# Kernel optimization log

Hardware: AMD Instinct MI355X
Metric: run time of the kernel (lower is better)

Reference implementation:

```python
import jax, jax.numpy as jnp
import numpy as np
import math

B, H, LQ, LK, D = 2, 16, 2048, 2048, 128

def setup_inputs() -> dict:
    key = jax.random.key(0)
    kq, kk, kv, km = jax.random.split(key, 4)
    return {
        "query": jax.random.normal(kq, (B, H, LQ, D), dtype=jnp.float32),
        "key": jax.random.normal(kk, (B, H, LK, D), dtype=jnp.float32),
        "value": jax.random.normal(kv, (B, H, LK, D), dtype=jnp.float32),
        # positive integer multiplicities in [1, 8] so log() is finite
        "key_multiplicities": jax.random.randint(km, (B, LK), 1, 9, dtype=jnp.int32),
    }

def reference(query, key, value, key_multiplicities):
    scale = 1.0 / math.sqrt(query.shape[-1])
    # scores: [B, H, Lq, Lk]
    scores = jnp.einsum("bhqd,bhkd->bhqk", query, key) * scale
    # additive log-multiplicity bias, broadcast over heads and queries
    log_mult = jnp.log(key_multiplicities.astype(scores.dtype))  # [B, Lk]
    scores = scores + log_mult[:, None, None, :]
    attn = jax.nn.softmax(scores, axis=-1)
    # dropout_p = 0.0 -> identity
    return jnp.einsum("bhqk,bhkd->bhqd", attn, value)
```

## Files before the change

### kernel.cpp

```cpp
#include <hip/hip_runtime.h>
#include <hip/hip_bf16.h>

constexpr int B_  = 2;
constexpr int H_  = 16;
constexpr int LQ_ = 2048;
constexpr int LK_ = 2048;
constexpr int D_  = 128;

constexpr int BM = 128;
constexpr int BN = 64;
constexpr int NT = LK_ / BN;
constexpr int TILE_SH = 64 * 128;

constexpr float SCALE_LOG2E = 0.12751649734586414f;

typedef short s16x4 __attribute__((ext_vector_type(4)));
typedef short s16x8 __attribute__((ext_vector_type(8)));
typedef float f32x4 __attribute__((ext_vector_type(4)));

#define MFMA16 __builtin_amdgcn_mfma_f32_16x16x32_bf16

#if __has_builtin(__builtin_amdgcn_exp2f)
#define EXP2(x) __builtin_amdgcn_exp2f(x)
#else
#define EXP2(x) exp2f(x)
#endif
#if __has_builtin(__builtin_amdgcn_logf)
#define LOG2(x) __builtin_amdgcn_logf(x)
#else
#define LOG2(x) log2f(x)
#endif

static __device__ __forceinline__ int pk2bf(float a, float b) {
  float2 t{a, b};
  __hip_bfloat162 h = __float22bfloat162_rn(t);
  return *reinterpret_cast<int*>(&h);
}

static __device__ __forceinline__ void dma16(const short* g, short* l) {
  __builtin_amdgcn_global_load_lds(
      (const __attribute__((address_space(1))) void*)g,
      (__attribute__((address_space(3))) void*)l, 16, 0, 0);
}

__global__ __launch_bounds__(256)
void prep(const float* __restrict__ kg, const float* __restrict__ vg,
          const int* __restrict__ multg, short* __restrict__ wsK,
          short* __restrict__ wsV, float* __restrict__ wsBias) {
  __shared__ float tileF[64 * 133];
  const int tid = threadIdx.x;
  const int wg  = blockIdx.x;
  const float* kp = kg + (size_t)wg * 64 * 128;
  const float* vp = vg + (size_t)wg * 64 * 128;
  short* wk = wsK + (size_t)wg * TILE_SH;
  short* wv = wsV + (size_t)wg * TILE_SH;

#pragma unroll
  for (int i = 0; i < 4; ++i) {
    int idx = tid + i * 256;
    int row = idx >> 4, blk = idx & 15;
    const float* src = kp + row * 128 + blk * 8;
    float4 a = *(const float4*)src;
    float4 c4 = *(const float4*)(src + 4);
    int4 t;
    t.x = pk2bf(a.x, a.y);  t.y = pk2bf(a.z, a.w);
    t.z = pk2bf(c4.x, c4.y); t.w = pk2bf(c4.z, c4.w);
    int pos = blk ^ (row & 15);
    *(int4*)&wk[row * 128 + pos * 8] = t;
  }

#pragma unroll
  for (int i = 0; i < 8; ++i) {
    int idx = tid + i * 256;
    int key = idx >> 5, d0 = (idx & 31) * 4;
    float4 a = *(const float4*)(vp + key * 128 + d0);
    float* dst = &tileF[key * 133 + d0];
    dst[0] = a.x; dst[1] = a.y; dst[2] = a.z; dst[3] = a.w;
  }
  __syncthreads();
#pragma unroll
  for (int i = 0; i < 4; ++i) {
    int idx = tid + i * 256;
    int d = idx >> 3, kgrp = idx & 7;
    float v[8];
#pragma unroll
    for (int j = 0; j < 8; ++j) v[j] = tileF[(kgrp * 8 + j) * 133 + d];
    int4 t;
    t.x = pk2bf(v[0], v[1]); t.y = pk2bf(v[2], v[3]);
    t.z = pk2bf(v[4], v[5]); t.w = pk2bf(v[6], v[7]);
    int pos = kgrp ^ ((d >> 1) & 7);
    *(int4*)&wv[d * 64 + pos * 8] = t;
  }

  if (wg < 8) {
    int b = wg >> 2;
    for (int j = tid; j < 512; j += 256) {
      int i0 = (wg & 3) * 512 + j;
      wsBias[b * LK_ + i0] = LOG2((float)multg[b * LK_ + i0]);
    }
  }
}

__global__ __launch_bounds__(256, 2)
void attn_fwd(const float* __restrict__ qg, const short* __restrict__ wsK,
              const short* __restrict__ wsV, const float* __restrict__ wsBias,
              float* __restrict__ outg) {
  __shared__ alignas(16) short Kbuf[2][TILE_SH];
  __shared__ alignas(16) short Vbuf[2][TILE_SH];
  __shared__ alignas(16) short Psh[128 * 64];

  const int tid  = threadIdx.x;
  const int w    = tid >> 6;
  const int lane = tid & 63;
  const int c    = lane & 15;
  const int qd   = lane >> 4;

  const int L   = blockIdx.y * gridDim.x + blockIdx.x;
  const int k8  = L >> 3;
  const int qb  = k8 & 15;
  const int bh  = (L & 7) * 4 + (k8 >> 4);
  const int b   = bh >> 4;

  const float* qptr = qg + (size_t)bh * LQ_ * D_;
  float*       optr = outg + (size_t)bh * LQ_ * D_;
  const short* kws  = wsK + (size_t)bh * NT * TILE_SH;
  const short* vws  = wsV + (size_t)bh * NT * TILE_SH;
  const float* bias = wsBias + b * LK_;

  const int q0 = qb * BM + w * 32;
  s16x8 qf[2][4];
#pragma unroll
  for (int qs = 0; qs < 2; ++qs) {
    const float* qrow = qptr + (size_t)(q0 + qs * 16 + c) * D_ + qd * 8;
#pragma unroll
    for (int kf = 0; kf < 4; ++kf) {
      float4 a  = *(const float4*)(qrow + kf * 32);
      float4 bq = *(const float4*)(qrow + kf * 32 + 4);
      int4 t;
      t.x = pk2bf(a.x * SCALE_LOG2E, a.y * SCALE_LOG2E);
      t.y = pk2bf(a.z * SCALE_LOG2E, a.w * SCALE_LOG2E);
      t.z = pk2bf(bq.x * SCALE_LOG2E, bq.y * SCALE_LOG2E);
      t.w = pk2bf(bq.z * SCALE_LOG2E, bq.w * SCALE_LOG2E);
      qf[qs][kf] = *(s16x8*)&t;
    }
  }

  f32x4 o[2][8];
  float m_r[2], l_r[2];
#pragma unroll
  for (int qs = 0; qs < 2; ++qs) {
#pragma unroll
    for (int dt = 0; dt < 8; ++dt) o[qs][dt] = (f32x4){0.f, 0.f, 0.f, 0.f};
    m_r[qs] = -INFINITY; l_r[qs] = 0.f;
  }

  auto dmaKV = [&](int kt, int bb) {
    const short* gK = kws + (size_t)kt * TILE_SH;
    const short* gV = vws + (size_t)kt * TILE_SH;
#pragma unroll
    for (int i = 0; i < 4; ++i) {
      int off = (w * 4 + i) * 512;
      dma16(gK + off + lane * 8, &Kbuf[bb][off]);
      dma16(gV + off + lane * 8, &Vbuf[bb][off]);
    }
  };

  dmaKV(0, 0);
  __syncthreads();

  for (int kt = 0; kt < NT; ++kt) {
    const int cur = kt & 1;
    if (kt + 1 < NT) dmaKV(kt + 1, cur ^ 1);

    float bvf[4][4];
#pragma unroll
    for (int ct = 0; ct < 4; ++ct) {
      float4 bv = *(const float4*)&bias[kt * BN + ct * 16 + qd * 4];
      bvf[ct][0] = bv.x; bvf[ct][1] = bv.y; bvf[ct][2] = bv.z; bvf[ct][3] = bv.w;
    }

    f32x4 St[2][4];
#pragma unroll
    for (int qs = 0; qs < 2; ++qs)
#pragma unroll
      for (int ct = 0; ct < 4; ++ct) St[qs][ct] = (f32x4){0.f, 0.f, 0.f, 0.f};

#pragma unroll
    for (int ct = 0; ct < 4; ++ct) {
      const short* kb = &Kbuf[cur][(ct * 16 + c) * 128];
#pragma unroll
      for (int kf = 0; kf < 4; ++kf) {
        s16x8 kfr = *(const s16x8*)&kb[((kf * 4 + qd) ^ c) * 8];
        St[0][ct] = MFMA16(kfr, qf[0][kf], St[0][ct], 0, 0, 0);
        St[1][ct] = MFMA16(kfr, qf[1][kf], St[1][ct], 0, 0, 0);
      }
    }

#pragma unroll
    for (int qs = 0; qs < 2; ++qs) {
      float x[4][4];
#pragma unroll
      for (int ct = 0; ct < 4; ++ct)
#pragma unroll
        for (int reg = 0; reg < 4; ++reg)
          x[ct][reg] = St[qs][ct][reg] + bvf[ct][reg];

      float mx = x[0][0];
#pragma unroll
      for (int ct = 0; ct < 4; ++ct)
#pragma unroll
        for (int reg = 0; reg < 4; ++reg) mx = fmaxf(mx, x[ct][reg]);
      mx = fmaxf(mx, __shfl_xor(mx, 16));
      mx = fmaxf(mx, __shfl_xor(mx, 32));

      float mn    = fmaxf(m_r[qs], mx);
      float alpha = EXP2(m_r[qs] - mn);
      m_r[qs] = mn;

      float rs = 0.f;
#pragma unroll
      for (int ct = 0; ct < 4; ++ct)
#pragma unroll
        for (int reg = 0; reg < 4; ++reg) {
          float p = EXP2(x[ct][reg] - mn);
          x[ct][reg] = p;
          rs += p;
        }
      rs += __shfl_xor(rs, 16);
      rs += __shfl_xor(rs, 32);
      l_r[qs] = l_r[qs] * alpha + rs;

      const int pr = w * 32 + qs * 16 + c;
#pragma unroll
      for (int ct = 0; ct < 4; ++ct) {
        int2 pk;
        pk.x = pk2bf(x[ct][0], x[ct][1]);
        pk.y = pk2bf(x[ct][2], x[ct][3]);
        int pos = (ct * 2 + (qd >> 1)) ^ (pr & 7);
        *(int2*)&Psh[pr * 64 + pos * 8 + (qd & 1) * 4] = pk;
      }

      float ar[4];
#pragma unroll
      for (int reg = 0; reg < 4; ++reg) ar[reg] = __shfl(alpha, qd * 4 + reg);
#pragma unroll
      for (int dt = 0; dt < 8; ++dt)
#pragma unroll
        for (int reg = 0; reg < 4; ++reg) o[qs][dt][reg] *= ar[reg];
    }

    s16x8 pf[2][2];
#pragma unroll
    for (int qs = 0; qs < 2; ++qs) {
      const int pr = w * 32 + qs * 16 + c;
#pragma unroll
      for (int kf = 0; kf < 2; ++kf) {
        int pos = (kf * 4 + qd) ^ (pr & 7);
        pf[qs][kf] = *(const s16x8*)&Psh[pr * 64 + pos * 8];
      }
    }
#pragma unroll
    for (int dt = 0; dt < 8; ++dt) {
      int d = dt * 16 + c;
      const short* vb = &Vbuf[cur][d * 64];
      s16x8 vf[2];
#pragma unroll
      for (int kf = 0; kf < 2; ++kf)
        vf[kf] = *(const s16x8*)&vb[((kf * 4 + qd) ^ ((d >> 1) & 7)) * 8];
#pragma unroll
      for (int qs = 0; qs < 2; ++qs)
#pragma unroll
        for (int kf = 0; kf < 2; ++kf)
          o[qs][dt] = MFMA16(pf[qs][kf], vf[kf], o[qs][dt], 0, 0, 0);
    }

    __syncthreads();
  }

#pragma unroll
  for (int qs = 0; qs < 2; ++qs) {
    float lr[4];
#pragma unroll
    for (int reg = 0; reg < 4; ++reg) lr[reg] = __shfl(l_r[qs], qd * 4 + reg);
#pragma unroll
    for (int reg = 0; reg < 4; ++reg) {
      float inv = 1.0f / lr[reg];
      int row = q0 + qs * 16 + qd * 4 + reg;
      float* orow = optr + (size_t)row * D_ + c;
#pragma unroll
      for (int dt = 0; dt < 8; ++dt) orow[dt * 16] = o[qs][dt][reg] * inv;
    }
  }
}

extern "C" void kernel_launch(void* const* d_in, const int* in_sizes, int n_in,
                              void* d_out, int out_size, void* d_ws, size_t ws_size,
                              hipStream_t stream) {
  const float* q = (const float*)d_in[0];
  const float* k = (const float*)d_in[1];
  const float* v = (const float*)d_in[2];
  const int* mult = (const int*)d_in[3];
  float* out = (float*)d_out;

  constexpr size_t KV_BYTES = (size_t)B_ * H_ * LK_ * D_ * 2;
  short* wsK = (short*)d_ws;
  short* wsV = (short*)((char*)d_ws + KV_BYTES);
  float* wsBias = (float*)((char*)d_ws + 2 * KV_BYTES);

  prep<<<dim3(B_ * H_ * NT), dim3(256), 0, stream>>>(k, v, mult, wsK, wsV, wsBias);

  dim3 grid(LQ_ / BM, B_ * H_);
  attn_fwd<<<grid, dim3(256), 0, stream>>>(q, wsK, wsV, wsBias, out);
}
```

Measured before the change: 231.9 us.

## Switch attention to 32x32x16 MFMA with register-resident P and lazy rescaling

Replaces the 16x16x32 MFMA tiling with 32x32x16 MFMAs, computing transposed scores so the probability tile can be turned into the PV operand with permlane32 swaps. This removes the shared-memory round trip for P. The bias is folded into the accumulator init. Output rescaling is skipped unless the running max grows by more than a threshold, which saves the multiply on most tiles at the cost of a looser numerical bound. MFMA sections are wrapped in s_setprio.

After: 213.9 us. 1.08x faster.

```diff
diff --git a/kernel.cpp b/kernel.cpp
--- a/kernel.cpp
+++ b/kernel.cpp
@@ -13,12 +13,12 @@
 constexpr int TILE_SH = 64 * 128;
 
 constexpr float SCALE_LOG2E = 0.12751649734586414f;
-
-typedef short s16x4 __attribute__((ext_vector_type(4)));
+constexpr float DEFER_THR   = 8.0f;
+
 typedef short s16x8 __attribute__((ext_vector_type(8)));
-typedef float f32x4 __attribute__((ext_vector_type(4)));
-
-#define MFMA16 __builtin_amdgcn_mfma_f32_16x16x32_bf16
+typedef float f32x16 __attribute__((ext_vector_type(16)));
+
+#define MFMA32 __builtin_amdgcn_mfma_f32_32x32x16_bf16
 
 #if __has_builtin(__builtin_amdgcn_exp2f)
 #define EXP2(x) __builtin_amdgcn_exp2f(x)
@@ -107,13 +107,12 @@
               float* __restrict__ outg) {
   __shared__ alignas(16) short Kbuf[2][TILE_SH];
   __shared__ alignas(16) short Vbuf[2][TILE_SH];
-  __shared__ alignas(16) short Psh[128 * 64];
 
   const int tid  = threadIdx.x;
   const int w    = tid >> 6;
   const int lane = tid & 63;
-  const int c    = lane & 15;
-  const int qd   = lane >> 4;
+  const int lq   = lane & 31;
+  const int hi   = lane >> 5;
 
   const int L   = blockIdx.y * gridDim.x + blockIdx.x;
   const int k8  = L >> 3;
@@ -128,31 +127,29 @@
   const float* bias = wsBias + b * LK_;
 
   const int q0 = qb * BM + w * 32;
-  s16x8 qf[2][4];
-#pragma unroll
-  for (int qs = 0; qs < 2; ++qs) {
-    const float* qrow = qptr + (size_t)(q0 + qs * 16 + c) * D_ + qd * 8;
-#pragma unroll
-    for (int kf = 0; kf < 4; ++kf) {
-      float4 a  = *(const float4*)(qrow + kf * 32);
-      float4 bq = *(const float4*)(qrow + kf * 32 + 4);
+
+  s16x8 qf[8];
+  {
+    const float* qrow = qptr + (size_t)(q0 + lq) * D_ + hi * 8;
+#pragma unroll
+    for (int kf = 0; kf < 8; ++kf) {
+      float4 a = *(const float4*)(qrow + kf * 16);
+      float4 c = *(const float4*)(qrow + kf * 16 + 4);
       int4 t;
       t.x = pk2bf(a.x * SCALE_LOG2E, a.y * SCALE_LOG2E);
       t.y = pk2bf(a.z * SCALE_LOG2E, a.w * SCALE_LOG2E);
-      t.z = pk2bf(bq.x * SCALE_LOG2E, bq.y * SCALE_LOG2E);
-      t.w = pk2bf(bq.z * SCALE_LOG2E, bq.w * SCALE_LOG2E);
-      qf[qs][kf] = *(s16x8*)&t;
-    }
-  }
-
-  f32x4 o[2][8];
-  float m_r[2], l_r[2];
-#pragma unroll
-  for (int qs = 0; qs < 2; ++qs) {
-#pragma unroll
-    for (int dt = 0; dt < 8; ++dt) o[qs][dt] = (f32x4){0.f, 0.f, 0.f, 0.f};
-    m_r[qs] = -INFINITY; l_r[qs] = 0.f;
-  }
+      t.z = pk2bf(c.x * SCALE_LOG2E, c.y * SCALE_LOG2E);
+      t.w = pk2bf(c.z * SCALE_LOG2E, c.w * SCALE_LOG2E);
+      qf[kf] = *(s16x8*)&t;
+    }
+  }
+
+  f32x16 o[4];
+#pragma unroll
+  for (int dt = 0; dt < 4; ++dt)
+#pragma unroll
+    for (int r = 0; r < 16; ++r) o[dt][r] = 0.f;
+  float m_r = -INFINITY, l_r = 0.f;
 
   auto dmaKV = [&](int kt, int bb) {
     const short* gK = kws + (size_t)kt * TILE_SH;
@@ -172,125 +169,113 @@
     const int cur = kt & 1;
     if (kt + 1 < NT) dmaKV(kt + 1, cur ^ 1);
 
-    float bvf[4][4];
-#pragma unroll
-    for (int ct = 0; ct < 4; ++ct) {
-      float4 bv = *(const float4*)&bias[kt * BN + ct * 16 + qd * 4];
-      bvf[ct][0] = bv.x; bvf[ct][1] = bv.y; bvf[ct][2] = bv.z; bvf[ct][3] = bv.w;
-    }
-
-    f32x4 St[2][4];
-#pragma unroll
-    for (int qs = 0; qs < 2; ++qs)
-#pragma unroll
-      for (int ct = 0; ct < 4; ++ct) St[qs][ct] = (f32x4){0.f, 0.f, 0.f, 0.f};
-
-#pragma unroll
-    for (int ct = 0; ct < 4; ++ct) {
-      const short* kb = &Kbuf[cur][(ct * 16 + c) * 128];
-#pragma unroll
-      for (int kf = 0; kf < 4; ++kf) {
-        s16x8 kfr = *(const s16x8*)&kb[((kf * 4 + qd) ^ c) * 8];
-        St[0][ct] = MFMA16(kfr, qf[0][kf], St[0][ct], 0, 0, 0);
-        St[1][ct] = MFMA16(kfr, qf[1][kf], St[1][ct], 0, 0, 0);
+    f32x16 St[2];
+#pragma unroll
+    for (int t = 0; t < 2; ++t)
+#pragma unroll
+      for (int g = 0; g < 4; ++g) {
+        float4 bv = *(const float4*)&bias[kt * BN + t * 32 + g * 8 + hi * 4];
+        St[t][g * 4 + 0] = bv.x; St[t][g * 4 + 1] = bv.y;
+        St[t][g * 4 + 2] = bv.z; St[t][g * 4 + 3] = bv.w;
       }
-    }
-
-#pragma unroll
-    for (int qs = 0; qs < 2; ++qs) {
-      float x[4][4];
-#pragma unroll
-      for (int ct = 0; ct < 4; ++ct)
-#pragma unroll
-        for (int reg = 0; reg < 4; ++reg)
-          x[ct][reg] = St[qs][ct][reg] + bvf[ct][reg];
-
-      float mx = x[0][0];
-#pragma unroll
-      for (int ct = 0; ct < 4; ++ct)
-#pragma unroll
-        for (int reg = 0; reg < 4; ++reg) mx = fmaxf(mx, x[ct][reg]);
-      mx = fmaxf(mx, __shfl_xor(mx, 16));
-      mx = fmaxf(mx, __shfl_xor(mx, 32));
-
-      float mn    = fmaxf(m_r[qs], mx);
-      float alpha = EXP2(m_r[qs] - mn);
-      m_r[qs] = mn;
-
-      float rs = 0.f;
-#pragma unroll
-      for (int ct = 0; ct < 4; ++ct)
-#pragma unroll
-        for (int reg = 0; reg < 4; ++reg) {
-          float p = EXP2(x[ct][reg] - mn);
-          x[ct][reg] = p;
-          rs += p;
+
+    __builtin_amdgcn_s_setprio(1);
+#pragma unroll
+    for (int t = 0; t < 2; ++t) {
+      const short* kb = &Kbuf[cur][(t * 32 + lq) * 128];
+#pragma unroll
+      for (int kf = 0; kf < 8; ++kf) {
+        s16x8 kfr = *(const s16x8*)&kb[((2 * kf + hi) ^ (lq & 15)) * 8];
+        St[t] = MFMA32(kfr, qf[kf], St[t], 0, 0, 0);
+      }
+    }
+    __builtin_amdgcn_s_setprio(0);
+
+    float t16[16];
+#pragma unroll
+    for (int i = 0; i < 16; ++i) t16[i] = fmaxf(St[0][i], St[1][i]);
+#pragma unroll
+    for (int s = 8; s >= 1; s >>= 1)
+#pragma unroll
+      for (int i = 0; i < s; ++i) t16[i] = fmaxf(t16[i], t16[i + s]);
+    float mx = fmaxf(t16[0], __shfl_xor(t16[0], 32));
+
+    if (__any(mx - m_r > DEFER_THR)) {
+      float mn    = fmaxf(m_r, mx);
+      float alpha = EXP2(m_r - mn);
+      m_r = mn;
+      l_r *= alpha;
+      float ar[16];
+#pragma unroll
+      for (int r = 0; r < 16; ++r)
+        ar[r] = __shfl(alpha, (r & 3) + 8 * (r >> 2) + 4 * hi);
+#pragma unroll
+      for (int dt = 0; dt < 4; ++dt)
+#pragma unroll
+        for (int r = 0; r < 16; ++r) o[dt][r] *= ar[r];
+    }
+
+    float px[2][16];
+#pragma unroll
+    for (int t = 0; t < 2; ++t)
+#pragma unroll
+      for (int r = 0; r < 16; ++r) px[t][r] = EXP2(St[t][r] - m_r);
+
+    float sa[16];
+#pragma unroll
+    for (int i = 0; i < 16; ++i) sa[i] = px[0][i] + px[1][i];
+#pragma unroll
+    for (int s = 8; s >= 1; s >>= 1)
+#pragma unroll
+      for (int i = 0; i < s; ++i) sa[i] += sa[i + s];
+    l_r += sa[0] + __shfl_xor(sa[0], 32);
+
+    s16x8 pf[2][2];
+#pragma unroll
+    for (int t = 0; t < 2; ++t) {
+      int P[8];
+#pragma unroll
+      for (int i = 0; i < 8; ++i) P[i] = pk2bf(px[t][2 * i], px[t][2 * i + 1]);
+#pragma unroll
+      for (int ks = 0; ks < 2; ++ks) {
+        int a0 = P[4 * ks + 0], a1 = P[4 * ks + 1];
+        int b0 = P[4 * ks + 2], b1 = P[4 * ks + 3];
+        asm("v_permlane32_swap_b32 %0, %1" : "+v"(a0), "+v"(b0));
+        asm("v_permlane32_swap_b32 %0, %1" : "+v"(a1), "+v"(b1));
+        int4 tt{a0, a1, b0, b1};
+        pf[t][ks] = *(s16x8*)&tt;
+      }
+    }
+
+    __builtin_amdgcn_s_setprio(1);
+#pragma unroll
+    for (int dt = 0; dt < 4; ++dt) {
+      const short* vb = &Vbuf[cur][(dt * 32 + lq) * 64];
+#pragma unroll
+      for (int t = 0; t < 2; ++t)
+#pragma unroll
+        for (int ks = 0; ks < 2; ++ks) {
+          s16x8 vf = *(const s16x8*)
+              &vb[((t * 4 + ks * 2 + hi) ^ ((lq >> 1) & 7)) * 8];
+          o[dt] = MFMA32(pf[t][ks], vf, o[dt], 0, 0, 0);
         }
-      rs += __shfl_xor(rs, 16);
-      rs += __shfl_xor(rs, 32);
-      l_r[qs] = l_r[qs] * alpha + rs;
-
-      const int pr = w * 32 + qs * 16 + c;
-#pragma unroll
-      for (int ct = 0; ct < 4; ++ct) {
-        int2 pk;
-        pk.x = pk2bf(x[ct][0], x[ct][1]);
-        pk.y = pk2bf(x[ct][2], x[ct][3]);
-        int pos = (ct * 2 + (qd >> 1)) ^ (pr & 7);
-        *(int2*)&Psh[pr * 64 + pos * 8 + (qd & 1) * 4] = pk;
-      }
-
-      float ar[4];
-#pragma unroll
-      for (int reg = 0; reg < 4; ++reg) ar[reg] = __shfl(alpha, qd * 4 + reg);
-#pragma unroll
-      for (int dt = 0; dt < 8; ++dt)
-#pragma unroll
-        for (int reg = 0; reg < 4; ++reg) o[qs][dt][reg] *= ar[reg];
-    }
-
-    s16x8 pf[2][2];
-#pragma unroll
-    for (int qs = 0; qs < 2; ++qs) {
-      const int pr = w * 32 + qs * 16 + c;
-#pragma unroll
-      for (int kf = 0; kf < 2; ++kf) {
-        int pos = (kf * 4 + qd) ^ (pr & 7);
-        pf[qs][kf] = *(const s16x8*)&Psh[pr * 64 + pos * 8];
-      }
-    }
-#pragma unroll
-    for (int dt = 0; dt < 8; ++dt) {
-      int d = dt * 16 + c;
-      const short* vb = &Vbuf[cur][d * 64];
-      s16x8 vf[2];
-#pragma unroll
-      for (int kf = 0; kf < 2; ++kf)
-        vf[kf] = *(const s16x8*)&vb[((kf * 4 + qd) ^ ((d >> 1) & 7)) * 8];
-#pragma unroll
-      for (int qs = 0; qs < 2; ++qs)
-#pragma unroll
-        for (int kf = 0; kf < 2; ++kf)
-          o[qs][dt] = MFMA16(pf[qs][kf], vf[kf], o[qs][dt], 0, 0, 0);
-    }
+    }
+    __builtin_amdgcn_s_setprio(0);
 
     __syncthreads();
   }
 
-#pragma unroll
-  for (int qs = 0; qs < 2; ++qs) {
-    float lr[4];
-#pragma unroll
-    for (int reg = 0; reg < 4; ++reg) lr[reg] = __shfl(l_r[qs], qd * 4 + reg);
-#pragma unroll
-    for (int reg = 0; reg < 4; ++reg) {
-      float inv = 1.0f / lr[reg];
-      int row = q0 + qs * 16 + qd * 4 + reg;
-      float* orow = optr + (size_t)row * D_ + c;
-#pragma unroll
-      for (int dt = 0; dt < 8; ++dt) orow[dt * 16] = o[qs][dt][reg] * inv;
-    }
-  }
+  float li[16];
+#pragma unroll
+  for (int r = 0; r < 16; ++r)
+    li[r] = 1.0f / __shfl(l_r, (r & 3) + 8 * (r >> 2) + 4 * hi);
+#pragma unroll
+  for (int dt = 0; dt < 4; ++dt)
+#pragma unroll
+    for (int r = 0; r < 16; ++r) {
+      int row = q0 + (r & 3) + 8 * (r >> 2) + 4 * hi;
+      optr[(size_t)row * D_ + dt * 32 + lq] = o[dt][r] * li[r];
+    }
 }
 
 extern "C" void kernel_launch(void* const* d_in, const int* in_sizes, int n_in,
```
